# Kernel tuning notes

Measured on AMD Instinct MI355X. Metric: run time of the kernel, lower is better.

## Reference

```python
import jax, jax.numpy as jnp
import numpy as np

N = 100000   # total nodes (users + items)
D = 256      # in_channels == out_channels
E = 1000000  # directed edges
C = 64       # number of clusters


def setup_inputs() -> dict:
    key = jax.random.key(0)
    k1, k2, k3, k4, k5 = jax.random.split(key, 5)
    X = jax.random.normal(k1, (N, D), jnp.float32)
    weight = jax.random.normal(k2, (D, D), jnp.float32) / np.sqrt(D).astype(np.float32)
    bias = jax.random.normal(k3, (D,), jnp.float32) * 0.01
    cluster_assignment = jax.random.randint(k4, (N,), 0, C)
    edge_index = jax.random.randint(k5, (2, E), 0, N)
    return {"X": X, "weight": weight, "bias": bias,
            "cluster_assignment": cluster_assignment, "edge_index": edge_index}


def reference(X, weight, bias, cluster_assignment, edge_index):
    # Per-cluster GCNConv == whole-graph GCNConv restricted to intra-cluster
    # edges (edges crossing clusters are masked out), with self-loops added
    # per node. Clusters with zero intra-cluster edges are skipped and keep
    # the original X (the Python loop `continue`s).
    src, dst = edge_index[0], edge_index[1]
    intra = (cluster_assignment[src] == cluster_assignment[dst]).astype(X.dtype)

    # GCN symmetric normalization with self-loops: deg = A_intra deg + 1
    deg = jax.ops.segment_sum(intra, dst, num_segments=N) + 1.0
    dinv = jax.lax.rsqrt(deg)                      # deg >= 1 always
    norm = dinv[src] * dinv[dst] * intra           # zero on cross-cluster edges

    Xl = X @ weight                                # [N, D] linear transform
    agg = jax.ops.segment_sum(norm[:, None] * Xl[src], dst, num_segments=N)
    agg = agg + (dinv * dinv)[:, None] * Xl        # self-loop contribution
    out = agg + bias

    # Clusters with no internal edges are left untouched by the torch loop.
    edges_per_cluster = jax.ops.segment_sum(intra, cluster_assignment[dst], num_segments=C)
    active = edges_per_cluster[cluster_assignment] > 0  # [N] bool
    return jnp.where(active[:, None], out, X)
```

## Files before the change

### kernel.cpp

```cpp
#include <hip/hip_runtime.h>

#define D 256

typedef float f32x4 __attribute__((ext_vector_type(4)));
typedef _Float16 f16x8 __attribute__((ext_vector_type(8)));

__global__ void k_edges(const int* __restrict__ ei, const int* __restrict__ cl,
                        float* __restrict__ degx, int E) {
    int e = blockIdx.x * blockDim.x + threadIdx.x;
    if (e >= E) return;
    int s = ei[e];
    int d = ei[E + e];
    if (cl[s] == cl[d])
        unsafeAtomicAdd(&degx[d], 1.0f);
}

__global__ void k_init(const float* __restrict__ X, const float* __restrict__ degx,
                       const int* __restrict__ cl, int* __restrict__ activeC,
                       float* __restrict__ out, int N) {
    int i = blockIdx.x * blockDim.x + threadIdx.x;
    int lane = threadIdx.x & 63;
    float dx = 0.0f;
    bool hit = false;
    if (i < N) {
        dx = degx[i];
        hit = dx > 0.0f;
        if (hit) activeC[cl[i]] = 1;
    }
    unsigned long long m = __ballot(hit);
    int base = i - lane;
    while (m) {
        int b = __ffsll((long long)m) - 1;
        m &= m - 1;
        int r = base + b;
        float inv = 1.0f / (__shfl(dx, b) + 1.0f);
        float4 x = *(const float4*)(X + (size_t)r * D + lane * 4);
        x.x *= inv; x.y *= inv; x.z *= inv; x.w *= inv;
        *(float4*)(out + (size_t)r * D + lane * 4) = x;
    }
}

__global__ void k_scatter(const int* __restrict__ ei, const int* __restrict__ cl,
                          const float* __restrict__ degx, const float* __restrict__ X,
                          float* __restrict__ out, int E) {
    int e = blockIdx.x * blockDim.x + threadIdx.x;
    int lane = threadIdx.x & 63;
    int s = 0, d = 0;
    bool intra = false;
    if (e < E) {
        s = ei[e];
        d = ei[E + e];
        intra = (cl[s] == cl[d]);
    }
    unsigned long long mask = __ballot(intra);
    while (mask) {
        int b = __ffsll((long long)mask) - 1;
        mask &= mask - 1;
        int ss = __shfl(s, b);
        int dd = __shfl(d, b);
        float norm = rsqrtf((degx[ss] + 1.0f) * (degx[dd] + 1.0f));
        float4 xv = *(const float4*)(X + (size_t)ss * D + lane * 4);
        float* op = out + (size_t)dd * D + lane * 4;
        unsafeAtomicAdd(op + 0, norm * xv.x);
        unsafeAtomicAdd(op + 1, norm * xv.y);
        unsafeAtomicAdd(op + 2, norm * xv.z);
        unsafeAtomicAdd(op + 3, norm * xv.w);
    }
}

__global__ void k_prepw(const float* __restrict__ W, _Float16* __restrict__ Wp) {
    int idx = blockIdx.x * blockDim.x + threadIdx.x;
    if (idx >= D * D) return;
    int k = idx >> 8, n = idx & 255;
    int ks = k >> 5, kk = k & 31;
    int h = kk >> 3, i = kk & 7;
    int ct = n >> 4, cn = n & 15;
    int lane = h * 16 + cn;
    Wp[(((ks * 16 + ct) * 64 + lane) << 3) + i] = (_Float16)W[idx];
}

__global__ __launch_bounds__(1024, 4) void k_gemm(
        const _Float16* __restrict__ Wp, const float* __restrict__ bias,
        const float* __restrict__ X, const float* __restrict__ degx,
        const int* __restrict__ cl, const int* __restrict__ activeC,
        float* __restrict__ out, int N) {
    extern __shared__ _Float16 Wl[];
    int tid  = threadIdx.x;
    int lane = tid & 63;
    int wid  = tid >> 6;
    int rA = lane & 15;
    int h  = lane >> 4;
    int cn = lane & 15;

    {
        const char* src = (const char*)Wp + tid * 16;
        #pragma unroll
        for (int it = 0; it < 8; ++it) {
            __builtin_amdgcn_global_load_lds(
                (const __attribute__((address_space(1))) void*)(src + it * 16384),
                (__attribute__((address_space(3))) void*)((char*)Wl + tid * 16 + it * 16384),
                16, 0, 0);
        }
    }
    float bv[16];
    #pragma unroll
    for (int ct = 0; ct < 16; ++ct) bv[ct] = bias[ct * 16 + cn];
    __syncthreads();

    int T = (N + 15) >> 4;
    for (int t = (int)blockIdx.x * 16 + wid; t < T; t += 4096) {
        long r = (long)t * 16 + rA;
        if (r > (long)N - 1) r = (long)N - 1;
        const float* arow = ((degx[r] > 0.0f) ? out : X) + r * D;

        f32x4 acc[16];
        #pragma unroll
        for (int ct = 0; ct < 16; ++ct) acc[ct] = (f32x4){0.f, 0.f, 0.f, 0.f};

        float4 Pa = *(const float4*)(arow + h * 8);
        float4 Pb = *(const float4*)(arow + h * 8 + 4);
        #pragma unroll
        for (int ks = 0; ks < 8; ++ks) {
            float4 a0 = Pa, a1 = Pb;
            if (ks < 7) {
                Pa = *(const float4*)(arow + (ks + 1) * 32 + h * 8);
                Pb = *(const float4*)(arow + (ks + 1) * 32 + h * 8 + 4);
            }
            f16x8 af;
            af[0]=(_Float16)a0.x; af[1]=(_Float16)a0.y; af[2]=(_Float16)a0.z; af[3]=(_Float16)a0.w;
            af[4]=(_Float16)a1.x; af[5]=(_Float16)a1.y; af[6]=(_Float16)a1.z; af[7]=(_Float16)a1.w;
            #pragma unroll
            for (int ct = 0; ct < 16; ++ct) {
                f16x8 wf = *(const f16x8*)&Wl[(((ks * 16 + ct) * 64) + lane) << 3];
                acc[ct] = __builtin_amdgcn_mfma_f32_16x16x32_f16(af, wf, acc[ct], 0, 0, 0);
            }
        }

        #pragma unroll
        for (int j = 0; j < 4; ++j) {
            long rr = (long)t * 16 + h * 4 + j;
            bool ok = rr < (long)N;
            long rc = ok ? rr : (long)N - 1;
            bool act = activeC[cl[rc]] != 0;
            unsigned long long bad = __ballot(!act || !ok);
            float* orow = out + rc * D;
            if (bad == 0ULL) {
                #pragma unroll
                for (int ct = 0; ct < 16; ++ct)
                    orow[ct * 16 + cn] = acc[ct][j] + bv[ct];
            } else if (ok) {
                const float* xrow = X + rc * D;
                #pragma unroll
                for (int ct = 0; ct < 16; ++ct) {
                    float v = acc[ct][j] + bv[ct];
                    if (!act) v = xrow[ct * 16 + cn];
                    orow[ct * 16 + cn] = v;
                }
            }
        }
    }
}

extern "C" void kernel_launch(void* const* d_in, const int* in_sizes, int n_in,
                              void* d_out, int out_size, void* d_ws, size_t ws_size,
                              hipStream_t stream) {
    const float* X    = (const float*)d_in[0];
    const float* W    = (const float*)d_in[1];
    const float* bias = (const float*)d_in[2];
    const int*   cl   = (const int*)d_in[3];
    const int*   ei   = (const int*)d_in[4];
    int N = in_sizes[3];
    int E = in_sizes[4] / 2;
    float* out = (float*)d_out;

    char* ws = (char*)d_ws;
    float* degx = (float*)ws;
    size_t off = ((size_t)N * sizeof(float) + 255) & ~(size_t)255;
    int* activeC = (int*)(ws + off);
    size_t zbytes = off + 256;
    _Float16* Wp = (_Float16*)(ws + ((zbytes + 255) & ~(size_t)255));

    hipFuncSetAttribute((const void*)k_gemm,
                        hipFuncAttributeMaxDynamicSharedMemorySize, 131072);

    hipMemsetAsync(ws, 0, zbytes, stream);
    k_prepw<<<(D * D + 255) / 256, 256, 0, stream>>>(W, Wp);
    k_edges<<<(E + 255) / 256, 256, 0, stream>>>(ei, cl, degx, E);
    k_init<<<(N + 255) / 256, 256, 0, stream>>>(X, degx, cl, activeC, out, N);
    k_scatter<<<(E + 255) / 256, 256, 0, stream>>>(ei, cl, degx, X, out, E);
    k_gemm<<<256, 1024, 131072, stream>>>(Wp, bias, X, degx, cl, activeC, out, N);
}
```

Before: 132.4 us.

## Prefetch next tile's full A row across GEMM iterations and fold memset into prep kernel

The GEMM loop now loads all 16 float4 of the next tile's A row, plus the degree value two tiles ahead, while it computes the current tile. Before, only one k-slice ahead was prefetched. This is meant to hide global-memory latency between tiles. Separately, the hipMemsetAsync is replaced by zeroing degx and activeC inside the weight-prep kernel, which drops one launch. The cost is 64 more VGPRs per thread for the prefetch buffer, which under launch_bounds(1024,4) risks spills or lower occupancy.

Result: slower. 204.1 us (+54.2%).

```diff
diff --git a/kernel.cpp b/kernel.cpp
--- a/kernel.cpp
+++ b/kernel.cpp
@@ -68,8 +68,12 @@
     }
 }
 
-__global__ void k_prepw(const float* __restrict__ W, _Float16* __restrict__ Wp) {
+__global__ void k_prepw(const float* __restrict__ W, _Float16* __restrict__ Wp,
+                        float* __restrict__ degx, int* __restrict__ activeC,
+                        int N) {
     int idx = blockIdx.x * blockDim.x + threadIdx.x;
+    if (idx < N) degx[idx] = 0.0f;
+    if (idx < 64) activeC[idx] = 0;
     if (idx >= D * D) return;
     int k = idx >> 8, n = idx & 255;
     int ks = k >> 5, kk = k & 31;
@@ -107,25 +111,43 @@
     for (int ct = 0; ct < 16; ++ct) bv[ct] = bias[ct * 16 + cn];
     __syncthreads();
 
-    int T = (N + 15) >> 4;
-    for (int t = (int)blockIdx.x * 16 + wid; t < T; t += 4096) {
-        long r = (long)t * 16 + rA;
-        if (r > (long)N - 1) r = (long)N - 1;
-        const float* arow = ((degx[r] > 0.0f) ? out : X) + r * D;
+    const int T = (N + 15) >> 4;
+    int t = (int)blockIdx.x * 16 + wid;
+    if (t >= T) return;
+
+    long r = (long)t * 16 + rA;
+    if (r > (long)N - 1) r = (long)N - 1;
+    const float* arow0 = ((degx[r] > 0.0f) ? out : X) + r * D;
+    float4 P[16];
+    #pragma unroll
+    for (int ks = 0; ks < 8; ++ks) {
+        P[2 * ks]     = *(const float4*)(arow0 + ks * 32 + h * 8);
+        P[2 * ks + 1] = *(const float4*)(arow0 + ks * 32 + h * 8 + 4);
+    }
+    int tn = t + 4096;
+    int tnc = (tn < T) ? tn : t;
+    long rn = (long)tnc * 16 + rA;
+    if (rn > (long)N - 1) rn = (long)N - 1;
+    float dgxN = degx[rn];
+
+    for (;;) {
+        const float* arowN = ((dgxN > 0.0f) ? out : X) + rn * D;
+
+        int t2 = t + 8192;
+        int t2c = (t2 < T) ? t2 : t;
+        long r2 = (long)t2c * 16 + rA;
+        if (r2 > (long)N - 1) r2 = (long)N - 1;
+        float dgx2 = degx[r2];
 
         f32x4 acc[16];
         #pragma unroll
         for (int ct = 0; ct < 16; ++ct) acc[ct] = (f32x4){0.f, 0.f, 0.f, 0.f};
 
-        float4 Pa = *(const float4*)(arow + h * 8);
-        float4 Pb = *(const float4*)(arow + h * 8 + 4);
         #pragma unroll
         for (int ks = 0; ks < 8; ++ks) {
-            float4 a0 = Pa, a1 = Pb;
-            if (ks < 7) {
-                Pa = *(const float4*)(arow + (ks + 1) * 32 + h * 8);
-                Pb = *(const float4*)(arow + (ks + 1) * 32 + h * 8 + 4);
-            }
+            float4 a0 = P[2 * ks], a1 = P[2 * ks + 1];
+            P[2 * ks]     = *(const float4*)(arowN + ks * 32 + h * 8);
+            P[2 * ks + 1] = *(const float4*)(arowN + ks * 32 + h * 8 + 4);
             f16x8 af;
             af[0]=(_Float16)a0.x; af[1]=(_Float16)a0.y; af[2]=(_Float16)a0.z; af[3]=(_Float16)a0.w;
             af[4]=(_Float16)a1.x; af[5]=(_Float16)a1.y; af[6]=(_Float16)a1.z; af[7]=(_Float16)a1.w;
@@ -158,6 +180,14 @@
                 }
             }
         }
+
+        if (tn >= T) break;
+        t = tn;
+        tn = t + 4096;
+        tnc = (tn < T) ? tn : t;
+        rn = (long)tnc * 16 + rA;
+        if (rn > (long)N - 1) rn = (long)N - 1;
+        dgxN = dgx2;
     }
 }
 
@@ -183,8 +213,8 @@
     hipFuncSetAttribute((const void*)k_gemm,
                         hipFuncAttributeMaxDynamicSharedMemorySize, 131072);
 
-    hipMemsetAsync(ws, 0, zbytes, stream);
-    k_prepw<<<(D * D + 255) / 256, 256, 0, stream>>>(W, Wp);
+    int npz = (N > D * D) ? N : D * D;
+    k_prepw<<<(npz + 255) / 256, 256, 0, stream>>>(W, Wp, degx, activeC, N);
     k_edges<<<(E + 255) / 256, 256, 0, stream>>>(ei, cl, degx, E);
     k_init<<<(N + 255) / 256, 256, 0, stream>>>(X, degx, cl, activeC, out, N);
     k_scatter<<<(E + 255) / 256, 256, 0, stream>>>(ei, cl, degx, X, out, E);
```
